# Optimization experiments

Measured on AMD Instinct MI355X. Metric: run time of the kernel, lower is better.

## Reference

```python
import jax, jax.numpy as jnp
import numpy as np

N = 12000
E = 384000
F_IN, F_HID, F_OUT = 4, 50, 1433
NEG_SLOPE = 0.2  # PyG GATConv default leaky_relu slope


def gat_conv(x, W, a_src, a_dst, b, src, dst):
    """PyG GATConv (heads=1, concat=True) with self-loops already appended.
    x: [N, Fin], W: [Fin, Fout], a_src/a_dst/b: [Fout], src/dst: [E']."""
    h = x @ W                                   # [N, Fout]
    al = h @ a_src                              # [N] per-source logit part
    ar = h @ a_dst                              # [N] per-target logit part
    e = jax.nn.leaky_relu(al[src] + ar[dst], NEG_SLOPE)   # [E'] edge logits
    # segment softmax over edges grouped by destination node
    m = jax.ops.segment_max(e, dst, num_segments=N)       # [N]
    ex = jnp.exp(e - m[dst])
    s = jax.ops.segment_sum(ex, dst, num_segments=N)      # [N]
    alpha = ex / s[dst]                         # [E'] (self-loops => s > 0)
    out = jax.ops.segment_sum(alpha[:, None] * h[src], dst, num_segments=N)
    return out + b


def setup_inputs() -> dict:
    key = jax.random.key(0)
    ks = jax.random.split(key, 10)
    x = jax.random.normal(ks[0], (N, F_IN), dtype=jnp.float32)
    edge_index = jax.random.randint(ks[1], (2, E), 0, N, dtype=jnp.int32)
    # Glorot-ish init for params
    W1 = jax.random.normal(ks[2], (F_IN, F_HID), dtype=jnp.float32) / np.sqrt(F_IN)
    a_src1 = jax.random.normal(ks[3], (F_HID,), dtype=jnp.float32) / np.sqrt(F_HID)
    a_dst1 = jax.random.normal(ks[4], (F_HID,), dtype=jnp.float32) / np.sqrt(F_HID)
    b1 = jnp.zeros((F_HID,), dtype=jnp.float32)
    W2 = jax.random.normal(ks[5], (F_HID, F_OUT), dtype=jnp.float32) / np.sqrt(F_HID)
    a_src2 = jax.random.normal(ks[6], (F_OUT,), dtype=jnp.float32) / np.sqrt(F_OUT)
    a_dst2 = jax.random.normal(ks[7], (F_OUT,), dtype=jnp.float32) / np.sqrt(F_OUT)
    b2 = jnp.zeros((F_OUT,), dtype=jnp.float32)
    return {"x": x, "edge_index": edge_index, "W1": W1, "a_src1": a_src1,
            "a_dst1": a_dst1, "b1": b1, "W2": W2, "a_src2": a_src2,
            "a_dst2": a_dst2, "b2": b2}


def reference(x, edge_index, W1, a_src1, a_dst1, b1, W2, a_src2, a_dst2, b2):
    # PyG GATConv adds self-loops by default
    loops = jnp.arange(N, dtype=edge_index.dtype)
    src = jnp.concatenate([edge_index[0], loops])
    dst = jnp.concatenate([edge_index[1], loops])
    h = jax.nn.relu(gat_conv(x, W1, a_src1, a_dst1, b1, src, dst))
    h = jax.nn.relu(gat_conv(h, W2, a_src2, a_dst2, b2, src, dst))
    adj_pred = jax.nn.sigmoid(h @ h.T)          # InnerProductDecoder.forward_all
    return (adj_pred, edge_index)
```

## Files before the change

kernel.cpp:

```cpp
#include <hip/hip_runtime.h>
#include <hip/hip_bf16.h>

#define NNODES 12000
#define NEDGES 384000
#define NETOT  (NEDGES + NNODES)
#define FIN    4
#define FHID   50
#define FOUT   1433
#define KP     1440
#define MP     12032
#define NEG_SLOPE 0.2f

typedef __hip_bfloat16 bf16_t;
typedef __bf16 bf16x8 __attribute__((ext_vector_type(8)));
typedef float  f32x4  __attribute__((ext_vector_type(4)));

__device__ __forceinline__ float  b2f(bf16_t h) { return __bfloat162float(h); }
__device__ __forceinline__ bf16_t f2b(float f)  { return __float2bfloat16(f); }
__device__ __forceinline__ float  blo(unsigned v) { union { unsigned u; float f; } c; c.u = v << 16; return c.f; }
__device__ __forceinline__ float  bhi(unsigned v) { union { unsigned u; float f; } c; c.u = v & 0xFFFF0000u; return c.f; }
__device__ __forceinline__ unsigned short f2bu(float f) { bf16_t h = f2b(f); return *(unsigned short*)&h; }

__global__ void k_init(int* __restrict__ deg, bf16_t* __restrict__ h2) {
    int i = blockIdx.x * blockDim.x + threadIdx.x;
    int stride = gridDim.x * blockDim.x;
    for (int v = i; v < NNODES; v += stride) deg[v] = 1;
    const size_t padN = (size_t)(MP - NNODES) * KP;
    for (size_t t = i; t < padN; t += stride) h2[(size_t)NNODES * KP + t] = f2b(0.f);
}

__global__ void k_count(const int* __restrict__ ei, int* __restrict__ deg) {
    int i = blockIdx.x * blockDim.x + threadIdx.x;
    if (i < NEDGES) atomicAdd(&deg[ei[NEDGES + i]], 1);
}

__global__ __launch_bounds__(1024) void k_scan(const int* __restrict__ deg, int* __restrict__ rowptr) {
    __shared__ int sd[1024];
    __shared__ int carry;
    int tid = threadIdx.x;
    if (tid == 0) { carry = 0; rowptr[0] = 0; }
    __syncthreads();
    for (int base = 0; base < NNODES; base += 1024) {
        int v = (base + tid < NNODES) ? deg[base + tid] : 0;
        sd[tid] = v;
        __syncthreads();
        for (int off = 1; off < 1024; off <<= 1) {
            int t = (tid >= off) ? sd[tid - off] : 0;
            __syncthreads();
            sd[tid] += t;
            __syncthreads();
        }
        int inc = sd[tid] + carry;
        if (base + tid < NNODES) rowptr[base + tid + 1] = inc;
        __syncthreads();
        if (tid == 1023) carry = sd[1023] + carry;
        __syncthreads();
    }
}

__global__ void k_cursor(const int* __restrict__ rowptr, int* __restrict__ cursor) {
    int i = blockIdx.x * blockDim.x + threadIdx.x;
    if (i < NNODES) cursor[i] = rowptr[i];
}

__global__ void k_fill(const int* __restrict__ ei, int* __restrict__ cursor, int* __restrict__ csrc) {
    int i = blockIdx.x * blockDim.x + threadIdx.x;
    if (i < NETOT) {
        int s, d;
        if (i < NEDGES) { s = ei[i]; d = ei[NEDGES + i]; }
        else            { s = d = i - NEDGES; }
        int pos = atomicAdd(&cursor[d], 1);
        csrc[pos] = s;
    }
}

__global__ __launch_bounds__(256) void k_linear1(
        const bf16_t* __restrict__ x, const bf16_t* __restrict__ W1,
        const bf16_t* __restrict__ as1, const bf16_t* __restrict__ ad1,
        float* __restrict__ h1pre, float* __restrict__ al, float* __restrict__ ar) {
    __shared__ float sW[FIN * FHID];
    __shared__ float sa[FHID], sdl[FHID];
    int tid = threadIdx.x;
    if (tid < FIN * FHID) sW[tid] = b2f(W1[tid]);
    if (tid < FHID) { sa[tid] = b2f(as1[tid]); sdl[tid] = b2f(ad1[tid]); }
    __syncthreads();
    int i = blockIdx.x * 256 + tid;
    if (i >= NNODES) return;
    float x0 = b2f(x[i * 4 + 0]), x1 = b2f(x[i * 4 + 1]);
    float x2 = b2f(x[i * 4 + 2]), x3 = b2f(x[i * 4 + 3]);
    float hal = 0.f, har = 0.f;
    for (int j = 0; j < FHID; ++j) {
        float h = x0 * sW[j] + x1 * sW[FHID + j] + x2 * sW[2 * FHID + j] + x3 * sW[3 * FHID + j];
        h1pre[(size_t)i * FHID + j] = h;
        hal += h * sa[j];
        har += h * sdl[j];
    }
    al[i] = hal; ar[i] = har;
}

__global__ __launch_bounds__(64) void k_agg1(
        const float* __restrict__ h1pre, const float* __restrict__ al, const float* __restrict__ ar,
        const int* __restrict__ rowptr, const int* __restrict__ csrc,
        const bf16_t* __restrict__ b1, float* __restrict__ h1) {
    int v = blockIdx.x, tid = threadIdx.x;
    int s0 = rowptr[v], s1 = rowptr[v + 1];
    float arv = ar[v];
    float m = -1e30f;
    for (int e = s0 + tid; e < s1; e += 64) {
        float l = al[csrc[e]] + arv;
        l = l > 0.f ? l : NEG_SLOPE * l;
        m = fmaxf(m, l);
    }
#pragma unroll
    for (int off = 32; off; off >>= 1) m = fmaxf(m, __shfl_xor(m, off, 64));
    __shared__ float sw[64];
    __shared__ int ssrc[64];
    float acc = 0.f, ssum = 0.f;
    for (int base = s0; base < s1; base += 64) {
        int e = base + tid;
        float w = 0.f; int si = 0;
        if (e < s1) {
            si = csrc[e];
            float l = al[si] + arv;
            l = l > 0.f ? l : NEG_SLOPE * l;
            w = __expf(l - m);
        }
        ssum += w;
        sw[tid] = w; ssrc[tid] = si;
        __syncthreads();
        int cnt = min(64, s1 - base);
        if (tid < FHID) {
            for (int j = 0; j < cnt; ++j)
                acc += sw[j] * h1pre[(size_t)ssrc[j] * FHID + tid];
        }
        __syncthreads();
    }
#pragma unroll
    for (int off = 32; off; off >>= 1) ssum += __shfl_xor(ssum, off, 64);
    if (tid < FHID) {
        float o = acc / ssum + b2f(b1[tid]);
        h1[(size_t)v * FHID + tid] = fmaxf(o, 0.f);
    }
}

__global__ __launch_bounds__(256) void k_linear2(
        const float* __restrict__ h1, const bf16_t* __restrict__ W2,
        const bf16_t* __restrict__ as2, const bf16_t* __restrict__ ad2,
        bf16_t* __restrict__ h2pre, float* __restrict__ al2, float* __restrict__ ar2) {
    int v0 = blockIdx.x * 4, tid = threadIdx.x;
    __shared__ float sh[4][FHID];
    if (tid < 4 * FHID) sh[tid / FHID][tid % FHID] = h1[(size_t)v0 * FHID + tid];
    __syncthreads();
    float pal[4] = {0.f, 0.f, 0.f, 0.f}, par[4] = {0.f, 0.f, 0.f, 0.f};
    for (int f = tid; f < KP; f += 256) {
        float a[4] = {0.f, 0.f, 0.f, 0.f};
        if (f < FOUT) {
#pragma unroll 10
            for (int k = 0; k < FHID; ++k) {
                float w = b2f(W2[k * FOUT + f]);
                a[0] += sh[0][k] * w; a[1] += sh[1][k] * w;
                a[2] += sh[2][k] * w; a[3] += sh[3][k] * w;
            }
            float sa = b2f(as2[f]), sd = b2f(ad2[f]);
#pragma unroll
            for (int c = 0; c < 4; ++c) { pal[c] += a[c] * sa; par[c] += a[c] * sd; }
        }
#pragma unroll
        for (int c = 0; c < 4; ++c) h2pre[(size_t)(v0 + c) * KP + f] = f2b(a[c]);
    }
#pragma unroll
    for (int off = 32; off; off >>= 1)
#pragma unroll
        for (int c = 0; c < 4; ++c) {
            pal[c] += __shfl_xor(pal[c], off, 64);
            par[c] += __shfl_xor(par[c], off, 64);
        }
    __shared__ float rA[4][4], rB[4][4];
    int wave = tid >> 6, lane = tid & 63;
    if (lane == 0)
#pragma unroll
        for (int c = 0; c < 4; ++c) { rA[wave][c] = pal[c]; rB[wave][c] = par[c]; }
    __syncthreads();
    if (tid < 4) {
        al2[v0 + tid] = rA[0][tid] + rA[1][tid] + rA[2][tid] + rA[3][tid];
        ar2[v0 + tid] = rB[0][tid] + rB[1][tid] + rB[2][tid] + rB[3][tid];
    }
}

__global__ __launch_bounds__(256) void k_agg2(
        const bf16_t* __restrict__ h2pre, const float* __restrict__ al, const float* __restrict__ ar,
        const int* __restrict__ rowptr, const int* __restrict__ csrc,
        const bf16_t* __restrict__ bias2, bf16_t* __restrict__ h2) {
    int v = blockIdx.x, tid = threadIdx.x;
    int s0 = rowptr[v], s1 = rowptr[v + 1];
    float arv = ar[v];
    float m = -1e30f;
    for (int e = s0 + tid; e < s1; e += 256) {
        float l = al[csrc[e]] + arv;
        l = l > 0.f ? l : NEG_SLOPE * l;
        m = fmaxf(m, l);
    }
#pragma unroll
    for (int off = 32; off; off >>= 1) m = fmaxf(m, __shfl_xor(m, off, 64));
    __shared__ float red[4];
    int wave = tid >> 6, lane = tid & 63;
    if (lane == 0) red[wave] = m;
    __syncthreads();
    m = fmaxf(fmaxf(red[0], red[1]), fmaxf(red[2], red[3]));
    __syncthreads();

    float a0 = 0.f, a1 = 0.f, a2 = 0.f, a3 = 0.f;
    float c0 = 0.f, c1 = 0.f, c2 = 0.f, c3 = 0.f;
    float ssum = 0.f;
    __shared__ float sw[256];
    __shared__ int ssrc[256];
    const bool hi = (tid < (360 - 256));
    for (int base = s0; base < s1; base += 256) {
        int e = base + tid;
        float w = 0.f; int si = 0;
        if (e < s1) {
            si = csrc[e];
            float l = al[si] + arv;
            l = l > 0.f ? l : NEG_SLOPE * l;
            w = __expf(l - m);
        }
        ssum += w;
        sw[tid] = w; ssrc[tid] = si;
        __syncthreads();
        int cnt = min(256, s1 - base);
#pragma unroll 4
        for (int j = 0; j < cnt; ++j) {
            float wj = sw[j];
            const uint2* hp = (const uint2*)(h2pre + (size_t)ssrc[j] * KP);
            uint2 p = hp[tid];
            a0 += wj * blo(p.x); a1 += wj * bhi(p.x);
            a2 += wj * blo(p.y); a3 += wj * bhi(p.y);
            if (hi) {
                uint2 q2 = hp[256 + tid];
                c0 += wj * blo(q2.x); c1 += wj * bhi(q2.x);
                c2 += wj * blo(q2.y); c3 += wj * bhi(q2.y);
            }
        }
        __syncthreads();
    }
#pragma unroll
    for (int off = 32; off; off >>= 1) ssum += __shfl_xor(ssum, off, 64);
    if (lane == 0) red[wave] = ssum;
    __syncthreads();
    float inv = 1.f / (red[0] + red[1] + red[2] + red[3]);

    {
        int fb = 4 * tid;
        ushort4 pk;
        pk.x = f2bu(fmaxf(a0 * inv + b2f(bias2[fb + 0]), 0.f));
        pk.y = f2bu(fmaxf(a1 * inv + b2f(bias2[fb + 1]), 0.f));
        pk.z = f2bu(fmaxf(a2 * inv + b2f(bias2[fb + 2]), 0.f));
        pk.w = f2bu(fmaxf(a3 * inv + b2f(bias2[fb + 3]), 0.f));
        *(ushort4*)(h2 + (size_t)v * KP + fb) = pk;
    }
    if (hi) {
        int fb = 1024 + 4 * tid;
        float vv[4] = {c0, c1, c2, c3};
        ushort4 pk;
        unsigned short* pp = (unsigned short*)&pk;
#pragma unroll
        for (int t = 0; t < 4; ++t) {
            int f = fb + t;
            float o = (f < FOUT) ? fmaxf(vv[t] * inv + b2f(bias2[f]), 0.f) : 0.f;
            pp[t] = f2bu(o);
        }
        *(ushort4*)(h2 + (size_t)v * KP + fb) = pk;
    }
}

__global__ __launch_bounds__(256) void k_gemm_sig(const bf16_t* __restrict__ Hm,
                                                  float* __restrict__ out) {
    const int bx = blockIdx.x, by = blockIdx.y;
    if (bx < by) return;
    __shared__ __align__(16) bf16_t As[128 * 32];
    __shared__ __align__(16) bf16_t Bs[128 * 32];
    const int tid = threadIdx.x;
    const int wave = tid >> 6;
    const int lane = tid & 63;
    const int rowA0 = by * 128;
    const int rowB0 = bx * 128;

    const int sRow  = wave * 16 + (lane >> 2);
    const int sSlot = (lane & 3) ^ ((lane >> 2) & 3);
    const bf16_t* gA = Hm + (size_t)(rowA0 + sRow) * KP + sSlot * 8;
    const bf16_t* gB = Hm + (size_t)(rowB0 + sRow) * KP + sSlot * 8;

    f32x4 acc[4][4] = {};

    const int wrow = wave >> 1, wcol = wave & 1;
    const int r = lane & 15, q = lane >> 4;
    const int rslot = q ^ (r & 3);
    const __bf16* Asb = (const __bf16*)As;
    const __bf16* Bsb = (const __bf16*)Bs;

    for (int kt = 0; kt < KP / 32; ++kt) {
        const int k0 = kt * 32;
#pragma unroll
        for (int c = 0; c < 2; ++c) {
            __builtin_amdgcn_global_load_lds(
                (const __attribute__((address_space(1))) void*)(gA + (size_t)c * 64 * KP + k0),
                (__attribute__((address_space(3))) void*)((char*)As + c * 4096 + wave * 1024),
                16, 0, 0);
            __builtin_amdgcn_global_load_lds(
                (const __attribute__((address_space(1))) void*)(gB + (size_t)c * 64 * KP + k0),
                (__attribute__((address_space(3))) void*)((char*)Bs + c * 4096 + wave * 1024),
                16, 0, 0);
        }
        __syncthreads();
        bf16x8 af[4], bfr[4];
#pragma unroll
        for (int mi = 0; mi < 4; ++mi)
            af[mi] = *(const bf16x8*)(Asb + ((wrow * 64 + mi * 16 + r) * 32 + rslot * 8));
#pragma unroll
        for (int ni = 0; ni < 4; ++ni)
            bfr[ni] = *(const bf16x8*)(Bsb + ((wcol * 64 + ni * 16 + r) * 32 + rslot * 8));
#pragma unroll
        for (int mi = 0; mi < 4; ++mi)
#pragma unroll
            for (int ni = 0; ni < 4; ++ni)
                acc[mi][ni] = __builtin_amdgcn_mfma_f32_16x16x32_bf16(af[mi], bfr[ni], acc[mi][ni], 0, 0, 0);
        __syncthreads();
    }

#pragma unroll
    for (int mi = 0; mi < 4; ++mi) {
        const int row0 = rowA0 + wrow * 64 + mi * 16 + q * 4;
#pragma unroll
        for (int ni = 0; ni < 4; ++ni) {
            const int col = rowB0 + wcol * 64 + ni * 16 + r;
            if (col < NNODES && row0 < NNODES) {
                f32x4 s;
#pragma unroll
                for (int r2 = 0; r2 < 4; ++r2)
                    s[r2] = 1.f / (1.f + __expf(-acc[mi][ni][r2]));
#pragma unroll
                for (int r2 = 0; r2 < 4; ++r2)
                    out[(size_t)(row0 + r2) * NNODES + col] = s[r2];
                if (bx != by)
                    *(f32x4*)(out + (size_t)col * NNODES + row0) = s;
            }
        }
    }
}

__global__ void k_edges(const int* __restrict__ ei, float* __restrict__ outbase) {
    int i = blockIdx.x * blockDim.x + threadIdx.x;
    if (i < 2 * NEDGES)
        outbase[(size_t)NNODES * (size_t)NNODES + (size_t)i] = (float)ei[i];
}

extern "C" void kernel_launch(void* const* d_in, const int* in_sizes, int n_in,
                              void* d_out, int out_size, void* d_ws, size_t ws_size,
                              hipStream_t stream) {
    const bf16_t* x   = (const bf16_t*)d_in[0];
    const int*    ei  = (const int*)d_in[1];
    const bf16_t* W1  = (const bf16_t*)d_in[2];
    const bf16_t* as1 = (const bf16_t*)d_in[3];
    const bf16_t* ad1 = (const bf16_t*)d_in[4];
    const bf16_t* b1  = (const bf16_t*)d_in[5];
    const bf16_t* W2  = (const bf16_t*)d_in[6];
    const bf16_t* as2 = (const bf16_t*)d_in[7];
    const bf16_t* ad2 = (const bf16_t*)d_in[8];
    const bf16_t* b2  = (const bf16_t*)d_in[9];
    float* out = (float*)d_out;

    char* obuf = (char*)d_out;
    size_t off = 0;
    auto carve = [&](size_t bytes) {
        char* p = obuf + off;
        off += (bytes + 255) & ~(size_t)255;
        return p;
    };
    float* h1pre  = (float*)carve((size_t)NNODES * FHID * 4);
    float* al1    = (float*)carve((size_t)NNODES * 4);
    float* ar1    = (float*)carve((size_t)NNODES * 4);
    float* h1     = (float*)carve((size_t)NNODES * FHID * 4);
    float* al2    = (float*)carve((size_t)NNODES * 4);
    float* ar2    = (float*)carve((size_t)NNODES * 4);
    int*   deg    = (int*)carve((size_t)NNODES * 4);
    int*   rowptr = (int*)carve((size_t)(NNODES + 1) * 4);
    int*   cursor = (int*)carve((size_t)NNODES * 4);
    int*   csrc   = (int*)carve((size_t)NETOT * 4);
    bf16_t* h2pre = (bf16_t*)carve((size_t)NNODES * KP * 2);
    bf16_t* h2 = (bf16_t*)d_ws;
    (void)ws_size; (void)in_sizes; (void)n_in; (void)out_size;

    hipLaunchKernelGGL(k_init,    dim3(256), dim3(256), 0, stream, deg, h2);
    hipLaunchKernelGGL(k_count,   dim3((NEDGES + 255) / 256), dim3(256), 0, stream, ei, deg);
    hipLaunchKernelGGL(k_scan,    dim3(1), dim3(1024), 0, stream, deg, rowptr);
    hipLaunchKernelGGL(k_cursor,  dim3((NNODES + 255) / 256), dim3(256), 0, stream, rowptr, cursor);
    hipLaunchKernelGGL(k_fill,    dim3((NETOT + 255) / 256), dim3(256), 0, stream, ei, cursor, csrc);
    hipLaunchKernelGGL(k_linear1, dim3((NNODES + 255) / 256), dim3(256), 0, stream,
                       x, W1, as1, ad1, h1pre, al1, ar1);
    hipLaunchKernelGGL(k_agg1,    dim3(NNODES), dim3(64), 0, stream,
                       h1pre, al1, ar1, rowptr, csrc, b1, h1);
    hipLaunchKernelGGL(k_linear2, dim3(NNODES / 4), dim3(256), 0, stream,
                       h1, W2, as2, ad2, h2pre, al2, ar2);
    hipLaunchKernelGGL(k_agg2,    dim3(NNODES), dim3(256), 0, stream,
                       h2pre, al2, ar2, rowptr, csrc, b2, h2);
    hipLaunchKernelGGL(k_gemm_sig, dim3(MP / 128, MP / 128), dim3(256), 0, stream, h2, out);
    hipLaunchKernelGGL(k_edges,   dim3((2 * NEDGES + 255) / 256), dim3(256), 0, stream, ei, out);
}
```

Measured before the change: 1.170 ms.

## Store layer-2 features in FP8 and use FP8 MFMA for decoder GEMM

Layer-2 pre-activations and the final hidden features are stored as FP8 instead of bf16, halving gather traffic in the aggregation and the bytes loaded by the inner-product GEMM. The GEMM switches to the 16x16x32 fp8 MFMA with a simpler LDS staging layout that drops the XOR swizzle. The FP8 precision loss may push the sigmoid outputs past tolerance, and the unswizzled LDS reads may cause bank conflicts. Also adds an unroll pragma to the layer-1 aggregation loop.

```diff
diff --git a/kernel.cpp b/kernel.cpp
--- a/kernel.cpp
+++ b/kernel.cpp
@@ -12,21 +12,18 @@
 #define NEG_SLOPE 0.2f
 
 typedef __hip_bfloat16 bf16_t;
-typedef __bf16 bf16x8 __attribute__((ext_vector_type(8)));
-typedef float  f32x4  __attribute__((ext_vector_type(4)));
+typedef float f32x4 __attribute__((ext_vector_type(4)));
+typedef float f32x2 __attribute__((ext_vector_type(2)));
 
 __device__ __forceinline__ float  b2f(bf16_t h) { return __bfloat162float(h); }
 __device__ __forceinline__ bf16_t f2b(float f)  { return __float2bfloat16(f); }
-__device__ __forceinline__ float  blo(unsigned v) { union { unsigned u; float f; } c; c.u = v << 16; return c.f; }
-__device__ __forceinline__ float  bhi(unsigned v) { union { unsigned u; float f; } c; c.u = v & 0xFFFF0000u; return c.f; }
-__device__ __forceinline__ unsigned short f2bu(float f) { bf16_t h = f2b(f); return *(unsigned short*)&h; }
-
-__global__ void k_init(int* __restrict__ deg, bf16_t* __restrict__ h2) {
+
+__global__ void k_init(int* __restrict__ deg, unsigned char* __restrict__ h2) {
     int i = blockIdx.x * blockDim.x + threadIdx.x;
     int stride = gridDim.x * blockDim.x;
     for (int v = i; v < NNODES; v += stride) deg[v] = 1;
     const size_t padN = (size_t)(MP - NNODES) * KP;
-    for (size_t t = i; t < padN; t += stride) h2[(size_t)NNODES * KP + t] = f2b(0.f);
+    for (size_t t = i; t < padN; t += stride) h2[(size_t)NNODES * KP + t] = 0;
 }
 
 __global__ void k_count(const int* __restrict__ ei, int* __restrict__ deg) {
@@ -130,6 +127,7 @@
         __syncthreads();
         int cnt = min(64, s1 - base);
         if (tid < FHID) {
+#pragma unroll 4
             for (int j = 0; j < cnt; ++j)
                 acc += sw[j] * h1pre[(size_t)ssrc[j] * FHID + tid];
         }
@@ -146,27 +144,46 @@
 __global__ __launch_bounds__(256) void k_linear2(
         const float* __restrict__ h1, const bf16_t* __restrict__ W2,
         const bf16_t* __restrict__ as2, const bf16_t* __restrict__ ad2,
-        bf16_t* __restrict__ h2pre, float* __restrict__ al2, float* __restrict__ ar2) {
+        unsigned char* __restrict__ h2pre, float* __restrict__ al2, float* __restrict__ ar2) {
     int v0 = blockIdx.x * 4, tid = threadIdx.x;
     __shared__ float sh[4][FHID];
     if (tid < 4 * FHID) sh[tid / FHID][tid % FHID] = h1[(size_t)v0 * FHID + tid];
     __syncthreads();
     float pal[4] = {0.f, 0.f, 0.f, 0.f}, par[4] = {0.f, 0.f, 0.f, 0.f};
-    for (int f = tid; f < KP; f += 256) {
-        float a[4] = {0.f, 0.f, 0.f, 0.f};
-        if (f < FOUT) {
+#pragma unroll
+    for (int i = 0; i < 3; ++i) {
+        int f0 = i * 512 + 2 * tid;
+        if (f0 < KP) {
+            float d0[4] = {0.f, 0.f, 0.f, 0.f}, d1[4] = {0.f, 0.f, 0.f, 0.f};
+            bool ok0 = f0 < FOUT, ok1 = f0 + 1 < FOUT;
+            if (ok0) {
+                int f1 = ok1 ? f0 + 1 : f0;
 #pragma unroll 10
-            for (int k = 0; k < FHID; ++k) {
-                float w = b2f(W2[k * FOUT + f]);
-                a[0] += sh[0][k] * w; a[1] += sh[1][k] * w;
-                a[2] += sh[2][k] * w; a[3] += sh[3][k] * w;
+                for (int k = 0; k < FHID; ++k) {
+                    float w0 = b2f(W2[k * FOUT + f0]);
+                    float w1 = b2f(W2[k * FOUT + f1]);
+#pragma unroll
+                    for (int c = 0; c < 4; ++c) {
+                        d0[c] += sh[c][k] * w0;
+                        d1[c] += sh[c][k] * w1;
+                    }
+                }
+                if (!ok1) { d1[0] = d1[1] = d1[2] = d1[3] = 0.f; }
+                float sa0 = b2f(as2[f0]), sd0 = b2f(ad2[f0]);
+                float sa1 = ok1 ? b2f(as2[f0 + 1]) : 0.f;
+                float sd1 = ok1 ? b2f(ad2[f0 + 1]) : 0.f;
+#pragma unroll
+                for (int c = 0; c < 4; ++c) {
+                    pal[c] += d0[c] * sa0 + d1[c] * sa1;
+                    par[c] += d0[c] * sd0 + d1[c] * sd1;
+                }
             }
-            float sa = b2f(as2[f]), sd = b2f(ad2[f]);
-#pragma unroll
-            for (int c = 0; c < 4; ++c) { pal[c] += a[c] * sa; par[c] += a[c] * sd; }
-        }
-#pragma unroll
-        for (int c = 0; c < 4; ++c) h2pre[(size_t)(v0 + c) * KP + f] = f2b(a[c]);
+#pragma unroll
+            for (int c = 0; c < 4; ++c) {
+                int pk = __builtin_amdgcn_cvt_pk_fp8_f32(d0[c], d1[c], 0, false);
+                *(unsigned short*)(h2pre + (size_t)(v0 + c) * KP + f0) = (unsigned short)pk;
+            }
+        }
     }
 #pragma unroll
     for (int off = 32; off; off >>= 1)
@@ -188,9 +205,9 @@
 }
 
 __global__ __launch_bounds__(256) void k_agg2(
-        const bf16_t* __restrict__ h2pre, const float* __restrict__ al, const float* __restrict__ ar,
+        const unsigned char* __restrict__ h2pre, const float* __restrict__ al, const float* __restrict__ ar,
         const int* __restrict__ rowptr, const int* __restrict__ csrc,
-        const bf16_t* __restrict__ bias2, bf16_t* __restrict__ h2) {
+        const bf16_t* __restrict__ bias2, unsigned char* __restrict__ h2) {
     int v = blockIdx.x, tid = threadIdx.x;
     int s0 = rowptr[v], s1 = rowptr[v + 1];
     float arv = ar[v];
@@ -209,12 +226,11 @@
     m = fmaxf(fmaxf(red[0], red[1]), fmaxf(red[2], red[3]));
     __syncthreads();
 
-    float a0 = 0.f, a1 = 0.f, a2 = 0.f, a3 = 0.f;
-    float c0 = 0.f, c1 = 0.f, c2 = 0.f, c3 = 0.f;
+    float acc[8] = {0.f, 0.f, 0.f, 0.f, 0.f, 0.f, 0.f, 0.f};
     float ssum = 0.f;
     __shared__ float sw[256];
     __shared__ int ssrc[256];
-    const bool hi = (tid < (360 - 256));
+    const bool act = tid < (KP / 8);
     for (int base = s0; base < s1; base += 256) {
         int e = base + tid;
         float w = 0.f; int si = 0;
@@ -228,17 +244,20 @@
         sw[tid] = w; ssrc[tid] = si;
         __syncthreads();
         int cnt = min(256, s1 - base);
+        if (act) {
 #pragma unroll 4
-        for (int j = 0; j < cnt; ++j) {
-            float wj = sw[j];
-            const uint2* hp = (const uint2*)(h2pre + (size_t)ssrc[j] * KP);
-            uint2 p = hp[tid];
-            a0 += wj * blo(p.x); a1 += wj * bhi(p.x);
-            a2 += wj * blo(p.y); a3 += wj * bhi(p.y);
-            if (hi) {
-                uint2 q2 = hp[256 + tid];
-                c0 += wj * blo(q2.x); c1 += wj * bhi(q2.x);
-                c2 += wj * blo(q2.y); c3 += wj * bhi(q2.y);
+            for (int j = 0; j < cnt; ++j) {
+                float wj = sw[j];
+                const uint2* hp = (const uint2*)(h2pre + (size_t)ssrc[j] * KP);
+                uint2 p = hp[tid];
+                f32x2 e0 = __builtin_amdgcn_cvt_pk_f32_fp8(p.x, false);
+                f32x2 e1 = __builtin_amdgcn_cvt_pk_f32_fp8(p.x, true);
+                f32x2 e2 = __builtin_amdgcn_cvt_pk_f32_fp8(p.y, false);
+                f32x2 e3 = __builtin_amdgcn_cvt_pk_f32_fp8(p.y, true);
+                acc[0] += wj * e0.x; acc[1] += wj * e0.y;
+                acc[2] += wj * e1.x; acc[3] += wj * e1.y;
+                acc[4] += wj * e2.x; acc[5] += wj * e2.y;
+                acc[6] += wj * e3.x; acc[7] += wj * e3.y;
             }
         }
         __syncthreads();
@@ -249,81 +268,67 @@
     __syncthreads();
     float inv = 1.f / (red[0] + red[1] + red[2] + red[3]);
 
-    {
-        int fb = 4 * tid;
-        ushort4 pk;
-        pk.x = f2bu(fmaxf(a0 * inv + b2f(bias2[fb + 0]), 0.f));
-        pk.y = f2bu(fmaxf(a1 * inv + b2f(bias2[fb + 1]), 0.f));
-        pk.z = f2bu(fmaxf(a2 * inv + b2f(bias2[fb + 2]), 0.f));
-        pk.w = f2bu(fmaxf(a3 * inv + b2f(bias2[fb + 3]), 0.f));
-        *(ushort4*)(h2 + (size_t)v * KP + fb) = pk;
-    }
-    if (hi) {
-        int fb = 1024 + 4 * tid;
-        float vv[4] = {c0, c1, c2, c3};
-        ushort4 pk;
-        unsigned short* pp = (unsigned short*)&pk;
-#pragma unroll
-        for (int t = 0; t < 4; ++t) {
+    if (act) {
+        int fb = 8 * tid;
+        float o[8];
+#pragma unroll
+        for (int t = 0; t < 8; ++t) {
             int f = fb + t;
-            float o = (f < FOUT) ? fmaxf(vv[t] * inv + b2f(bias2[f]), 0.f) : 0.f;
-            pp[t] = f2bu(o);
-        }
-        *(ushort4*)(h2 + (size_t)v * KP + fb) = pk;
-    }
-}
-
-__global__ __launch_bounds__(256) void k_gemm_sig(const bf16_t* __restrict__ Hm,
+            o[t] = (f < FOUT) ? fmaxf(acc[t] * inv + b2f(bias2[f]), 0.f) : 0.f;
+        }
+        uint2 pk;
+        int w0 = __builtin_amdgcn_cvt_pk_fp8_f32(o[0], o[1], 0, false);
+        pk.x = (unsigned)__builtin_amdgcn_cvt_pk_fp8_f32(o[2], o[3], w0, true);
+        int w1 = __builtin_amdgcn_cvt_pk_fp8_f32(o[4], o[5], 0, false);
+        pk.y = (unsigned)__builtin_amdgcn_cvt_pk_fp8_f32(o[6], o[7], w1, true);
+        *(uint2*)(h2 + (size_t)v * KP + fb) = pk;
+    }
+}
+
+__global__ __launch_bounds__(256) void k_gemm_sig(const unsigned char* __restrict__ Hm,
                                                   float* __restrict__ out) {
     const int bx = blockIdx.x, by = blockIdx.y;
     if (bx < by) return;
-    __shared__ __align__(16) bf16_t As[128 * 32];
-    __shared__ __align__(16) bf16_t Bs[128 * 32];
+    __shared__ __align__(16) unsigned char As[128 * 32];
+    __shared__ __align__(16) unsigned char Bs[128 * 32];
     const int tid = threadIdx.x;
     const int wave = tid >> 6;
     const int lane = tid & 63;
     const int rowA0 = by * 128;
     const int rowB0 = bx * 128;
 
-    const int sRow  = wave * 16 + (lane >> 2);
-    const int sSlot = (lane & 3) ^ ((lane >> 2) & 3);
-    const bf16_t* gA = Hm + (size_t)(rowA0 + sRow) * KP + sSlot * 8;
-    const bf16_t* gB = Hm + (size_t)(rowB0 + sRow) * KP + sSlot * 8;
+    const int sRow = wave * 32 + (lane >> 1);
+    const int sOff = (lane & 1) * 16;
+    const unsigned char* gA = Hm + (size_t)(rowA0 + sRow) * KP + sOff;
+    const unsigned char* gB = Hm + (size_t)(rowB0 + sRow) * KP + sOff;
+    const int ldsOff = wave * 1024 + lane * 16;
 
     f32x4 acc[4][4] = {};
 
     const int wrow = wave >> 1, wcol = wave & 1;
     const int r = lane & 15, q = lane >> 4;
-    const int rslot = q ^ (r & 3);
-    const __bf16* Asb = (const __bf16*)As;
-    const __bf16* Bsb = (const __bf16*)Bs;
 
     for (int kt = 0; kt < KP / 32; ++kt) {
         const int k0 = kt * 32;
-#pragma unroll
-        for (int c = 0; c < 2; ++c) {
-            __builtin_amdgcn_global_load_lds(
-                (const __attribute__((address_space(1))) void*)(gA + (size_t)c * 64 * KP + k0),
-                (__attribute__((address_space(3))) void*)((char*)As + c * 4096 + wave * 1024),
-                16, 0, 0);
-            __builtin_amdgcn_global_load_lds(
-                (const __attribute__((address_space(1))) void*)(gB + (size_t)c * 64 * KP + k0),
-                (__attribute__((address_space(3))) void*)((char*)Bs + c * 4096 + wave * 1024),
-                16, 0, 0);
-        }
-        __syncthreads();
-        bf16x8 af[4], bfr[4];
+        __builtin_amdgcn_global_load_lds(
+            (const __attribute__((address_space(1))) void*)(gA + k0),
+            (__attribute__((address_space(3))) void*)(As + ldsOff), 16, 0, 0);
+        __builtin_amdgcn_global_load_lds(
+            (const __attribute__((address_space(1))) void*)(gB + k0),
+            (__attribute__((address_space(3))) void*)(Bs + ldsOff), 16, 0, 0);
+        __syncthreads();
+        long af[4], bfr[4];
 #pragma unroll
         for (int mi = 0; mi < 4; ++mi)
-            af[mi] = *(const bf16x8*)(Asb + ((wrow * 64 + mi * 16 + r) * 32 + rslot * 8));
+            af[mi] = *(const long*)(As + (wrow * 64 + mi * 16 + r) * 32 + q * 8);
 #pragma unroll
         for (int ni = 0; ni < 4; ++ni)
-            bfr[ni] = *(const bf16x8*)(Bsb + ((wcol * 64 + ni * 16 + r) * 32 + rslot * 8));
+            bfr[ni] = *(const long*)(Bs + (wcol * 64 + ni * 16 + r) * 32 + q * 8);
 #pragma unroll
         for (int mi = 0; mi < 4; ++mi)
 #pragma unroll
             for (int ni = 0; ni < 4; ++ni)
-                acc[mi][ni] = __builtin_amdgcn_mfma_f32_16x16x32_bf16(af[mi], bfr[ni], acc[mi][ni], 0, 0, 0);
+                acc[mi][ni] = __builtin_amdgcn_mfma_f32_16x16x32_fp8_fp8(af[mi], bfr[ni], acc[mi][ni], 0, 0, 0);
         __syncthreads();
     }
 
@@ -386,8 +391,8 @@
     int*   rowptr = (int*)carve((size_t)(NNODES + 1) * 4);
     int*   cursor = (int*)carve((size_t)NNODES * 4);
     int*   csrc   = (int*)carve((size_t)NETOT * 4);
-    bf16_t* h2pre = (bf16_t*)carve((size_t)NNODES * KP * 2);
-    bf16_t* h2 = (bf16_t*)d_ws;
+    unsigned char* h2pre = (unsigned char*)carve((size_t)NNODES * KP);
+    unsigned char* h2 = (unsigned char*)d_ws;
     (void)ws_size; (void)in_sizes; (void)n_in; (void)out_size;
 
     hipLaunchKernelGGL(k_init,    dim3(256), dim3(256), 0, stream, deg, h2);
```

After: 1.257 ms. +7.4%, slower.
